# Kernel optimization log

Hardware: AMD Instinct MI355X
Metric: run time of the kernel (lower is better)

The kernel has to match this reference:

```python
import jax, jax.numpy as jnp
import numpy as np

C, H, W = 32, 128, 128

def grid_sample_plane(plane, gx, gy):
    """PyTorch F.grid_sample(mode='bilinear', align_corners=True, padding_mode='zeros').
    plane: (C,H,W); gx,gy: (B,N) in [-1,1] (x indexes W, y indexes H).
    Returns (B,C,N)."""
    x = (gx + 1.0) * 0.5 * (W - 1)
    y = (gy + 1.0) * 0.5 * (H - 1)
    x0 = jnp.floor(x); y0 = jnp.floor(y)
    wx = x - x0; wy = y - y0
    x0i = x0.astype(jnp.int32); y0i = y0.astype(jnp.int32)
    def corner(xi, yi, w):
        valid = (xi >= 0) & (xi < W) & (yi >= 0) & (yi < H)
        xc = jnp.clip(xi, 0, W - 1); yc = jnp.clip(yi, 0, H - 1)
        v = plane[:, yc, xc]            # (C,B,N)
        return v * (w * valid)[None]
    out = (corner(x0i, y0i, (1 - wx) * (1 - wy))
           + corner(x0i + 1, y0i, wx * (1 - wy))
           + corner(x0i, y0i + 1, (1 - wx) * wy)
           + corner(x0i + 1, y0i + 1, wx * wy))   # (C,B,N)
    return jnp.transpose(out, (1, 0, 2))           # (B,C,N)


def setup_inputs() -> dict:
    key = jax.random.key(0)
    ks = jax.random.split(key, 8)
    B, N = 4, 262144
    grid_coords = jax.random.uniform(ks[0], (B, N, 3), jnp.float32, -1.0, 1.0)
    triplanes = jax.random.normal(ks[1], (3 * C, H, W), jnp.float32)
    w0 = jax.random.normal(ks[2], (128, 32), jnp.float32) * (1.0 / np.sqrt(32))
    b0 = jax.random.normal(ks[3], (128,), jnp.float32) * 0.01
    w1 = jax.random.normal(ks[4], (128, 128), jnp.float32) * (1.0 / np.sqrt(128))
    b1 = jax.random.normal(ks[5], (128,), jnp.float32) * 0.01
    w2 = jax.random.normal(ks[6], (4, 128), jnp.float32) * (1.0 / np.sqrt(128))
    b2 = jax.random.normal(ks[7], (4,), jnp.float32) * 0.01
    return {"grid_coords": grid_coords, "triplanes": triplanes,
            "w0": w0, "b0": b0, "w1": w1, "b1": b1, "w2": w2, "b2": b2}


def reference(grid_coords, triplanes, w0, b0, w1, b1, w2, b2):
    B, N, _ = grid_coords.shape
    feat_xy, feat_yz, feat_xz = jnp.split(triplanes, 3, axis=0)
    x = grid_coords[..., 0]; y = grid_coords[..., 1]; z = grid_coords[..., 2]
    # fused tri-plane gather + sum, (B,C,N)
    sampled = (grid_sample_plane(feat_xy, x, y)
               + grid_sample_plane(feat_xz, x, z)
               + grid_sample_plane(feat_yz, y, z))
    # NOTE: the original code does .reshape(batch, -1, channel) on a (B,C,1,N)
    # contiguous tensor (NOT a transpose) -- replicate that exact layout reinterpretation.
    feats = sampled.reshape(B, N, C)
    net = jax.nn.relu(feats @ w0.T + b0)
    net = jax.nn.relu(net @ w1.T + b1)
    net = jax.nn.relu(net @ w2.T + b2)            # (B,N,4)
    # raw = cat(rgb=net[...,1:4], alpha=net[...,0:1]) along channel
    raw = jnp.concatenate([net[..., 1:4], net[..., 0:1]], axis=-1)
    return raw
```

## Files before the change

kernel.cpp:

```cpp
#include <hip/hip_runtime.h>
#include <hip/hip_bf16.h>


#define C_ 32
#define HW_ (128 * 128)
#define HBS2 136

typedef short s8v __attribute__((ext_vector_type(8)));
typedef float f4v __attribute__((ext_vector_type(4)));
typedef unsigned int u4v __attribute__((ext_vector_type(4)));
typedef unsigned int u2v __attribute__((ext_vector_type(2)));

__device__ __attribute__((aligned(64))) unsigned short g_planes[3 * HW_ * C_];
__device__ __attribute__((aligned(16))) unsigned short g_w0[128 * 32];
__device__ __attribute__((aligned(16))) unsigned short g_w1[128 * 128];
__device__ __attribute__((aligned(16))) unsigned short g_w2[16 * 128];
__device__ __attribute__((aligned(16))) float g_b0[128];
__device__ __attribute__((aligned(16))) float g_b1[128];
__device__ __attribute__((aligned(16))) float g_b2p[16];

template <typename TO, typename FROM>
static __device__ __forceinline__ TO bitc(FROM f) {
    union { FROM a; TO b; } u; u.a = f; return u.b;
}

template <typename V>
static __device__ __forceinline__ auto mfma_k32(V a, V b, f4v c, int)
    -> decltype(__builtin_amdgcn_mfma_f32_16x16x32_bf16(a, b, c, 0, 0, 0)) {
    return __builtin_amdgcn_mfma_f32_16x16x32_bf16(a, b, c, 0, 0, 0);
}
template <typename V>
static __device__ __forceinline__ f4v mfma_k32(V a, V b, f4v c, long) {
    typedef __bf16 b8v __attribute__((ext_vector_type(8)));
    return __builtin_amdgcn_mfma_f32_16x16x32_bf16(bitc<b8v>(a), bitc<b8v>(b), c, 0, 0, 0);
}
static __device__ __forceinline__ f4v MFMA(s8v a, s8v b, f4v c) {
    return mfma_k32(a, b, c, 0);
}

__device__ __forceinline__ unsigned short f2bf(float f) {
    union { float f; unsigned int i; } v; v.f = f;
    unsigned int r = v.i + 0x7FFFu + ((v.i >> 16) & 1u);
    return (unsigned short)(r >> 16);
}

static __device__ __forceinline__ unsigned int relu_pk(float a, float b) {
    float x = a > 0.0f ? a : 0.0f;
    float y = b > 0.0f ? b : 0.0f;
    unsigned int r;
    asm("v_cvt_pk_bf16_f32 %0, %1, %2" : "=v"(r) : "v"(x), "v"(y));
    return r;
}

#define LGKM0() do { asm volatile("s_waitcnt lgkmcnt(0)" ::: "memory"); \
                     __builtin_amdgcn_sched_barrier(0); } while (0)

__global__ __launch_bounds__(256) void prep_planes_k(const float* __restrict__ tp) {
    __shared__ float buf[32][65];
    const int tid = threadIdx.x;
    const int bid = blockIdx.x;
    const int pl  = bid >> 8;
    const int xy0 = (bid & 255) << 6;
#pragma unroll
    for (int i = 0; i < 8; ++i) {
        int idx = i * 256 + tid;
        int c = idx >> 6, x = idx & 63;
        buf[c][x] = tp[(pl * C_ + c) * HW_ + xy0 + x];
    }
    __syncthreads();
#pragma unroll
    for (int i = 0; i < 8; ++i) {
        int idx = i * 256 + tid;
        int x = idx >> 5, c = idx & 31;
        g_planes[(pl * HW_ + xy0 + x) * C_ + c] = f2bf(buf[c][x]);
    }
}

__global__ void prep_weights_k(const float* __restrict__ w0, const float* __restrict__ b0,
                               const float* __restrict__ w1, const float* __restrict__ b1,
                               const float* __restrict__ w2, const float* __restrict__ b2) {
    int i = blockIdx.x * 256 + threadIdx.x;
    if (i < 128 * 32)  g_w0[i] = f2bf(w0[i]);
    if (i < 128 * 128) g_w1[i] = f2bf(w1[i]);
    if (i < 16 * 128) {
        int n = i >> 7, k = i & 127;
        g_w2[i] = f2bf(n < 4 ? w2[((n + 1) & 3) * 128 + k] : 0.0f);
    }
    if (i < 128) { g_b0[i] = b0[i]; g_b1[i] = b1[i]; }
    if (i < 16)  g_b2p[i] = (i < 4) ? b2[(i + 1) & 3] : 0.0f;
}

__device__ __forceinline__ void sample_plane32(const unsigned short* __restrict__ pbase,
                                               float u, float v, float* facc) {
    float x = (u + 1.0f) * 63.5f;
    float y = (v + 1.0f) * 63.5f;
    float xf = floorf(x), yf = floorf(y);
    float wx = x - xf, wy = y - yf;
    int x0 = (int)xf, y0 = (int)yf;
#pragma unroll
    for (int dy = 0; dy < 2; ++dy) {
        int yi = y0 + dy;
        float wyv = dy ? wy : 1.0f - wy;
        bool vy = (yi >= 0) && (yi < 128);
        int yc = yi < 0 ? 0 : (yi > 127 ? 127 : yi);
#pragma unroll
        for (int dx = 0; dx < 2; ++dx) {
            int xi = x0 + dx;
            float wv = (dx ? wx : 1.0f - wx) * wyv;
            bool vx = (xi >= 0) && (xi < 128);
            int xc = xi < 0 ? 0 : (xi > 127 ? 127 : xi);
            wv = (vx && vy) ? wv : 0.0f;
            const u4v* cp = (const u4v*)(pbase + (yc * 128 + xc) * C_);
#pragma unroll
            for (int q = 0; q < 4; ++q) {
                u4v dw = cp[q];
#pragma unroll
                for (int jj = 0; jj < 4; ++jj) {
                    facc[q * 8 + 2 * jj]     += wv * __uint_as_float(dw[jj] << 16);
                    facc[q * 8 + 2 * jj + 1] += wv * __uint_as_float(dw[jj] & 0xFFFF0000u);
                }
            }
        }
    }
}

__global__ __launch_bounds__(256) void fused_k(const float* __restrict__ coords,
                                               float* __restrict__ out) {
    __shared__ __attribute__((aligned(16))) unsigned short smem[16384 + 4 * 16 * HBS2];
    __shared__ __attribute__((aligned(16))) float lds_bias[256];
    const int tid  = threadIdx.x;
    const int wave = tid >> 6;
    const int lane = tid & 63;
    const int l15  = lane & 15;
    const int quad = lane >> 4;
    const int ch8  = quad * 8;

    const int wg = blockIdx.x;
    const int b  = wg >> 9;
    const int nb = wg & 511;
    const int n0 = nb << 9;

    if (tid < 128) { lds_bias[tid] = g_b0[tid]; lds_bias[128 + tid] = g_b1[tid]; }

#pragma unroll 1
    for (int pt = 0; pt < 2; ++pt) {
        const int nl = tid + pt * 256;
        const float* cp = coords + (size_t)(b * 262144 + n0 + nl) * 3;
        const float gx = cp[0], gy = cp[1], gz = cp[2];
        float facc[32];
#pragma unroll
        for (int c = 0; c < 32; ++c) facc[c] = 0.0f;
        sample_plane32(g_planes + 0 * (HW_ * C_), gx, gy, facc);
        sample_plane32(g_planes + 2 * (HW_ * C_), gx, gz, facc);
        sample_plane32(g_planes + 1 * (HW_ * C_), gy, gz, facc);
#pragma unroll
        for (int c = 0; c < 32; ++c)
            smem[c * 512 + nl] = f2bf(facc[c]);
    }
    __syncthreads();

    s8v w0f[8], w1f[4][8], w2f[4];
#pragma unroll
    for (int nt = 0; nt < 8; ++nt)
        w0f[nt] = *(const s8v*)(g_w0 + (nt * 16 + l15) * 32 + ch8);
#pragma unroll
    for (int kc = 0; kc < 4; ++kc)
#pragma unroll
        for (int nt = 0; nt < 8; ++nt)
            w1f[kc][nt] = *(const s8v*)(g_w1 + (nt * 16 + l15) * 128 + kc * 32 + ch8);
#pragma unroll
    for (int kc = 0; kc < 4; ++kc)
        w2f[kc] = *(const s8v*)(g_w2 + l15 * 128 + kc * 32 + ch8);
    const f4v b2v = *(const f4v*)(g_b2p + quad * 4);

    unsigned short* hb = smem + 16384 + wave * (16 * HBS2);

#pragma unroll 1
    for (int i = 0; i < 8; ++i) {
        const int ci = wave * 8 + i;
        int bo = 0;
        asm volatile("" : "+v"(bo));
        const float* bp = lds_bias + bo;

        const s8v a = *(const s8v*)(smem + ci * 512 + l15 * 32 + ch8);

#pragma unroll
        for (int nt = 0; nt < 8; ++nt) {
            const f4v bi = *(const f4v*)(bp + nt * 16 + quad * 4);
            f4v c1 = MFMA(w0f[nt], a, bi);
            u2v pk;
            pk[0] = relu_pk(c1[0], c1[1]);
            pk[1] = relu_pk(c1[2], c1[3]);
            *(u2v*)(hb + l15 * HBS2 + nt * 16 + quad * 4) = pk;
        }
        LGKM0();
        s8v a2[4];
#pragma unroll
        for (int kc = 0; kc < 4; ++kc)
            a2[kc] = *(const s8v*)(hb + l15 * HBS2 + kc * 32 + ch8);

#pragma unroll
        for (int half = 0; half < 2; ++half) {
            f4v d[4];
#pragma unroll
            for (int j = 0; j < 4; ++j)
                d[j] = *(const f4v*)(bp + 128 + (half * 4 + j) * 16 + quad * 4);
#pragma unroll
            for (int kc = 0; kc < 4; ++kc)
#pragma unroll
                for (int j = 0; j < 4; ++j)
                    d[j] = MFMA(w1f[kc][half * 4 + j], a2[kc], d[j]);
#pragma unroll
            for (int j = 0; j < 4; ++j) {
                u2v pk;
                pk[0] = relu_pk(d[j][0], d[j][1]);
                pk[1] = relu_pk(d[j][2], d[j][3]);
                *(u2v*)(hb + l15 * HBS2 + (half * 4 + j) * 16 + quad * 4) = pk;
            }
        }
        LGKM0();
        s8v a3[4];
#pragma unroll
        for (int kc = 0; kc < 4; ++kc)
            a3[kc] = *(const s8v*)(hb + l15 * HBS2 + kc * 32 + ch8);

        f4v o = b2v;
#pragma unroll
        for (int kc = 0; kc < 4; ++kc)
            o = MFMA(w2f[kc], a3[kc], o);

        if (quad == 0) {
            f4v r;
#pragma unroll
            for (int j = 0; j < 4; ++j) r[j] = o[j] > 0.0f ? o[j] : 0.0f;
            const int t = b * 16384 + ci * 512 + nb;
            *(f4v*)(out + (size_t)(t * 16 + l15) * 4) = r;
        }
    }
}

extern "C" void kernel_launch(void* const* d_in, const int* in_sizes, int n_in,
                              void* d_out, int out_size, void* d_ws, size_t ws_size,
                              hipStream_t stream) {
    const float* coords = (const float*)d_in[0];
    const float* tp = (const float*)d_in[1];
    const float* w0 = (const float*)d_in[2];
    const float* b0 = (const float*)d_in[3];
    const float* w1 = (const float*)d_in[4];
    const float* b1 = (const float*)d_in[5];
    const float* w2 = (const float*)d_in[6];
    const float* b2 = (const float*)d_in[7];
    float* out = (float*)d_out;

    prep_planes_k<<<768, 256, 0, stream>>>(tp);
    prep_weights_k<<<64, 256, 0, stream>>>(w0, b0, w1, b1, w2, b2);
    fused_k<<<2048, 256, 0, stream>>>(coords, out);
}
```

Baseline: 219.1 us.

## Interleave MLP layers per 32-wide K chunk with a small LDS staging buffer

Restructures the per-tile MLP so each 32-channel chunk of the layer-0 output is written to a small per-wave LDS buffer and fed straight into the layer-1 MFMAs, instead of materialising the full 128-wide hidden activation first. Layer-2 is handled the same way, consuming layer-1 outputs chunk by chunk. This cuts the LDS scratch per wave from 136 to 40 halfwords per row and removes the explicit lgkmcnt waits and schedule barriers, leaving the compiler to handle ordering. It also adds a launch-bounds occupancy hint of 4 blocks. The risks are more frequent short LDS round trips on the critical path, possible hazards now that the explicit waits are gone, and extra register pressure from keeping eight accumulators live.

```diff
diff --git a/kernel.cpp b/kernel.cpp
--- a/kernel.cpp
+++ b/kernel.cpp
@@ -4,7 +4,7 @@
 
 #define C_ 32
 #define HW_ (128 * 128)
-#define HBS2 136
+#define HQS 40
 
 typedef short s8v __attribute__((ext_vector_type(8)));
 typedef float f4v __attribute__((ext_vector_type(4)));
@@ -51,9 +51,6 @@
     asm("v_cvt_pk_bf16_f32 %0, %1, %2" : "=v"(r) : "v"(x), "v"(y));
     return r;
 }
-
-#define LGKM0() do { asm volatile("s_waitcnt lgkmcnt(0)" ::: "memory"); \
-                     __builtin_amdgcn_sched_barrier(0); } while (0)
 
 __global__ __launch_bounds__(256) void prep_planes_k(const float* __restrict__ tp) {
     __shared__ float buf[32][65];
@@ -124,9 +121,9 @@
     }
 }
 
-__global__ __launch_bounds__(256) void fused_k(const float* __restrict__ coords,
-                                               float* __restrict__ out) {
-    __shared__ __attribute__((aligned(16))) unsigned short smem[16384 + 4 * 16 * HBS2];
+__global__ __launch_bounds__(256, 4) void fused_k(const float* __restrict__ coords,
+                                                  float* __restrict__ out) {
+    __shared__ __attribute__((aligned(16))) unsigned short smem[16384 + 4 * 16 * HQS];
     __shared__ __attribute__((aligned(16))) float lds_bias[256];
     const int tid  = threadIdx.x;
     const int wave = tid >> 6;
@@ -173,7 +170,7 @@
         w2f[kc] = *(const s8v*)(g_w2 + l15 * 128 + kc * 32 + ch8);
     const f4v b2v = *(const f4v*)(g_b2p + quad * 4);
 
-    unsigned short* hb = smem + 16384 + wave * (16 * HBS2);
+    unsigned short* hbq = smem + 16384 + wave * (16 * HQS);
 
 #pragma unroll 1
     for (int i = 0; i < 8; ++i) {
@@ -184,50 +181,43 @@
 
         const s8v a = *(const s8v*)(smem + ci * 512 + l15 * 32 + ch8);
 
-#pragma unroll
-        for (int nt = 0; nt < 8; ++nt) {
-            const f4v bi = *(const f4v*)(bp + nt * 16 + quad * 4);
-            f4v c1 = MFMA(w0f[nt], a, bi);
-            u2v pk;
-            pk[0] = relu_pk(c1[0], c1[1]);
-            pk[1] = relu_pk(c1[2], c1[3]);
-            *(u2v*)(hb + l15 * HBS2 + nt * 16 + quad * 4) = pk;
-        }
-        LGKM0();
-        s8v a2[4];
-#pragma unroll
-        for (int kc = 0; kc < 4; ++kc)
-            a2[kc] = *(const s8v*)(hb + l15 * HBS2 + kc * 32 + ch8);
-
-#pragma unroll
-        for (int half = 0; half < 2; ++half) {
-            f4v d[4];
-#pragma unroll
-            for (int j = 0; j < 4; ++j)
-                d[j] = *(const f4v*)(bp + 128 + (half * 4 + j) * 16 + quad * 4);
-#pragma unroll
-            for (int kc = 0; kc < 4; ++kc)
-#pragma unroll
-                for (int j = 0; j < 4; ++j)
-                    d[j] = MFMA(w1f[kc][half * 4 + j], a2[kc], d[j]);
-#pragma unroll
-            for (int j = 0; j < 4; ++j) {
+        f4v d[8];
+#pragma unroll
+        for (int j = 0; j < 8; ++j)
+            d[j] = *(const f4v*)(bp + 128 + j * 16 + quad * 4);
+
+#pragma unroll
+        for (int kc = 0; kc < 4; ++kc) {
+#pragma unroll
+            for (int s = 0; s < 2; ++s) {
+                const int nt = 2 * kc + s;
+                const f4v bi = *(const f4v*)(bp + nt * 16 + quad * 4);
+                f4v c1 = MFMA(w0f[nt], a, bi);
+                u2v pk;
+                pk[0] = relu_pk(c1[0], c1[1]);
+                pk[1] = relu_pk(c1[2], c1[3]);
+                *(u2v*)(hbq + l15 * HQS + s * 16 + quad * 4) = pk;
+            }
+            const s8v a2 = *(const s8v*)(hbq + l15 * HQS + ch8);
+#pragma unroll
+            for (int j = 0; j < 8; ++j)
+                d[j] = MFMA(w1f[kc][j], a2, d[j]);
+        }
+
+        f4v o = b2v;
+#pragma unroll
+        for (int kc = 0; kc < 4; ++kc) {
+#pragma unroll
+            for (int s = 0; s < 2; ++s) {
+                const int j = 2 * kc + s;
                 u2v pk;
                 pk[0] = relu_pk(d[j][0], d[j][1]);
                 pk[1] = relu_pk(d[j][2], d[j][3]);
-                *(u2v*)(hb + l15 * HBS2 + (half * 4 + j) * 16 + quad * 4) = pk;
+                *(u2v*)(hbq + l15 * HQS + s * 16 + quad * 4) = pk;
             }
-        }
-        LGKM0();
-        s8v a3[4];
-#pragma unroll
-        for (int kc = 0; kc < 4; ++kc)
-            a3[kc] = *(const s8v*)(hb + l15 * HBS2 + kc * 32 + ch8);
-
-        f4v o = b2v;
-#pragma unroll
-        for (int kc = 0; kc < 4; ++kc)
-            o = MFMA(w2f[kc], a3[kc], o);
+            const s8v a3 = *(const s8v*)(hbq + l15 * HQS + ch8);
+            o = MFMA(w2f[kc], a3, o);
+        }
 
         if (quad == 0) {
             f4v r;
```

New measurement: 465.9 us. 113% more time.
